# Kernel optimization log

Measured on AMD Instinct MI355X. Metric: run time of the kernel, lower is better.

The kernel has to match this reference:

```python
import jax, jax.numpy as jnp
import numpy as np

NUM_CLASSES = 2
THRESHOLD = 0.35
NEGPOS_RATIO = 7
VARIANCES = (0.1, 0.2)
B, P, O = 64, 16800, 64  # batch, num_priors, num_objs per image


def point_form(pr):
    # cxcywh -> xyxy
    return jnp.concatenate([pr[:, :2] - pr[:, 2:] / 2, pr[:, :2] + pr[:, 2:] / 2], axis=1)


def jaccard(a, b):
    # a: [A,4] xyxy, b: [Bx,4] xyxy -> IoU [A,Bx]
    lt = jnp.maximum(a[:, None, :2], b[None, :, :2])
    rb = jnp.minimum(a[:, None, 2:], b[None, :, 2:])
    wh = jnp.clip(rb - lt, 0.0)
    inter = wh[..., 0] * wh[..., 1]
    area_a = ((a[:, 2] - a[:, 0]) * (a[:, 3] - a[:, 1]))[:, None]
    area_b = ((b[:, 2] - b[:, 0]) * (b[:, 3] - b[:, 1]))[None, :]
    return inter / (area_a + area_b - inter)


def encode(matched, priors):
    # matched xyxy [P,4], priors cxcywh [P,4]
    g_cxcy = (matched[:, :2] + matched[:, 2:]) / 2 - priors[:, :2]
    g_cxcy = g_cxcy / (VARIANCES[0] * priors[:, 2:])
    g_wh = (matched[:, 2:] - matched[:, :2]) / priors[:, 2:]
    g_wh = jnp.log(g_wh) / VARIANCES[1]
    return jnp.concatenate([g_cxcy, g_wh], axis=1)


def encode_landm(matched, priors):
    # matched [P,10] -> [P,5,2]
    m = matched.reshape(-1, 5, 2)
    g = (m - priors[:, None, :2]) / (VARIANCES[0] * priors[:, None, 2:])
    return g.reshape(-1, 10)


def match_one(truths, labels, landms, priors):
    # truths [O,4], labels [O], landms [O,10]
    overlaps = jaccard(truths, point_form(priors))  # [O,P]
    best_prior_overlap = overlaps.max(axis=1)       # per-gt best IoU
    best_prior_idx = overlaps.argmax(axis=1)
    valid_gt = best_prior_overlap >= 0.2
    best_truth_overlap = overlaps.max(axis=0)       # per-prior best IoU
    best_truth_idx = overlaps.argmax(axis=0)
    # index_fill(2) only for valid gts (best_prior_idx_filter)
    bto = best_truth_overlap.at[best_prior_idx].set(
        jnp.where(valid_gt, 2.0, best_truth_overlap[best_prior_idx]))
    # ensure every gt keeps its best prior
    bti = best_truth_idx.at[best_prior_idx].set(jnp.arange(truths.shape[0]))
    matches = truths[bti]                  # [P,4]
    conf = labels[bti]                     # [P]
    conf = jnp.where(bto < THRESHOLD, 0.0, conf)
    loc = encode(matches, priors)
    landm = encode_landm(landms[bti], priors)
    return loc, conf, landm


def smooth_l1_sum(x, mask):
    ax = jnp.abs(x)
    v = jnp.where(ax < 1.0, 0.5 * ax * ax, ax - 0.5)
    return (v * mask).sum()


def setup_inputs() -> dict:
    key = jax.random.key(0)
    k1, k2, k3, k4, k5, k6, k7, k8 = jax.random.split(key, 8)
    loc_data = jax.random.normal(k1, (B, P, 4), jnp.float32)
    conf_data = jax.random.normal(k2, (B, P, NUM_CLASSES), jnp.float32)
    landm_data = jax.random.normal(k3, (B, P, 10), jnp.float32)
    # priors: cx,cy in (0,1), w,h in (0.02,0.22)
    cxy = jax.random.uniform(k4, (P, 2), jnp.float32)
    wh = jax.random.uniform(k5, (P, 2), jnp.float32) * 0.2 + 0.02
    priors = jnp.concatenate([cxy, wh], axis=1)
    # targets: valid corner boxes + landmarks + label in {1,-1}
    xy1 = jax.random.uniform(k6, (B, O, 2), jnp.float32) * 0.6
    bwh = jax.random.uniform(k7, (B, O, 2), jnp.float32) * 0.3 + 0.05
    boxes = jnp.concatenate([xy1, xy1 + bwh], axis=-1)
    lms = jax.random.uniform(k8, (B, O, 10), jnp.float32)
    lab = jnp.where(jax.random.uniform(jax.random.fold_in(key, 9), (B, O, 1)) < 0.3, -1.0, 1.0)
    targets = jnp.concatenate([boxes, lms, lab], axis=-1)
    return {"loc_data": loc_data, "conf_data": conf_data, "landm_data": landm_data,
            "priors": priors, "targets": targets}


def reference(loc_data, conf_data, landm_data, priors, targets):
    num = loc_data.shape[0]
    num_priors = priors.shape[0]
    truths = targets[:, :, :4]
    landms = targets[:, :, 4:14]
    labels = targets[:, :, -1]
    loc_t, conf_t, landm_t = jax.vmap(match_one, in_axes=(0, 0, 0, None))(
        truths, labels, landms, priors)  # [B,P,4], [B,P], [B,P,10]

    # landmark loss over conf_t > 0
    pos1 = conf_t > 0
    num_pos_landm = pos1.astype(jnp.int32).sum(axis=1, keepdims=True)
    N1 = jnp.maximum(num_pos_landm.sum().astype(jnp.float32), 1.0)
    loss_landm = smooth_l1_sum(landm_data - landm_t, pos1[..., None].astype(landm_data.dtype))

    # localization loss over conf_t != 0 ; conf_t[pos] = 1
    pos = conf_t != 0
    conf_t01 = jnp.where(pos, 1, 0)  # int {0,1}
    loss_l = smooth_l1_sum(loc_data - loc_t, pos[..., None].astype(loc_data.dtype))

    # hard negative mining on per-prior CE loss (global-max log_sum_exp, as in source)
    batch_conf = conf_data.reshape(-1, NUM_CLASSES)
    x_max = batch_conf.max()
    lse = jnp.log(jnp.exp(batch_conf - x_max).sum(axis=1, keepdims=True)) + x_max
    gathered = jnp.take_along_axis(batch_conf, conf_t01.reshape(-1, 1), axis=1)
    loss_c = (lse - gathered).reshape(num, -1)  # [B,P]; positives NOT zeroed (as in source)
    loss_idx = jnp.argsort(-loss_c, axis=1)
    idx_rank = jnp.argsort(loss_idx, axis=1)
    num_pos = pos.astype(jnp.int32).sum(axis=1, keepdims=True)  # [B,1]
    num_neg = jnp.minimum(NEGPOS_RATIO * num_pos, num_priors - 1)
    neg = idx_rank < num_neg  # [B,P]
    neg_pos = pos | neg

    # cross-entropy (sum) over selected pos+neg priors
    logp = jax.nn.log_softmax(conf_data, axis=-1)  # [B,P,C]
    ce = -jnp.take_along_axis(logp, conf_t01[..., None], axis=-1)[..., 0]
    loss_c_final = (ce * neg_pos.astype(ce.dtype)).sum()

    N = jnp.maximum(num_pos.sum().astype(jnp.float32), 1.0)
    return (loss_l / N, loss_c_final / N, loss_landm / N1)
```

## Files before the change

kernel.cpp:

```cpp
#include <hip/hip_runtime.h>
#include <math.h>

#define BN 64
#define PN 16800
#define ON 64
#define THRESH 0.35f
#define NEGPOS 7
#define GX 66
#define NBLK (BN * GX)
#define GXB 33
#define NB_BT (BN * GXB)
#define TG 4

__device__ __forceinline__ unsigned f2key(float f) {
  unsigned u = __float_as_uint(f);
  return (u & 0x80000000u) ? ~u : (u | 0x80000000u);
}
__device__ __forceinline__ float key2f(unsigned k) {
  unsigned u = (k & 0x80000000u) ? (k & 0x7FFFFFFFu) : ~k;
  return __uint_as_float(u);
}

struct Acc {
  unsigned xmax_key;
};

__device__ __forceinline__ float sl1(float d) {
  float a = fabsf(d);
  return (a < 1.f) ? 0.5f * a * a : a - 0.5f;
}

__global__ void k_best_truth(const float* __restrict__ priors,
                             const float* __restrict__ targets,
                             const float* __restrict__ conf,
                             float* __restrict__ bto, int* __restrict__ bti,
                             unsigned* __restrict__ bmax) {
  int b = blockIdx.y;
  int tid = threadIdx.x;
  int p0 = blockIdx.x * 512 + tid;
  int p1 = p0 + 256;
  bool v1 = p1 < PN;

  __shared__ float4 tbox[ON];
  __shared__ float tarea[ON];
  if (tid < ON) {
    const float* tg = &targets[((long)b * ON + tid) * 15];
    float4 bx = make_float4(tg[0], tg[1], tg[2], tg[3]);
    tbox[tid] = bx;
    tarea[tid] = (bx.z - bx.x) * (bx.w - bx.y);
  }
  __syncthreads();

  float2 c0 = reinterpret_cast<const float2*>(conf)[(long)b * PN + p0];
  float cmax = fmaxf(c0.x, c0.y);
  if (v1) {
    float2 c1 = reinterpret_cast<const float2*>(conf)[(long)b * PN + p1];
    cmax = fmaxf(cmax, fmaxf(c1.x, c1.y));
  }

  float4 prA = reinterpret_cast<const float4*>(priors)[p0];
  float4 prB = reinterpret_cast<const float4*>(priors)[v1 ? p1 : p0];
  float ax1A = prA.x - prA.z * 0.5f, ay1A = prA.y - prA.w * 0.5f;
  float ax2A = prA.x + prA.z * 0.5f, ay2A = prA.y + prA.w * 0.5f;
  float abA = (ax2A - ax1A) * (ay2A - ay1A);
  float ax1B = prB.x - prB.z * 0.5f, ay1B = prB.y - prB.w * 0.5f;
  float ax2B = prB.x + prB.z * 0.5f, ay2B = prB.y + prB.w * 0.5f;
  float abB = (ax2B - ax1B) * (ay2B - ay1B);

  float biA = -1.f, buA = 1.f, biB = -1.f, buB = 1.f;
  int idA = 0, idB = 0;
#pragma unroll 4
  for (int t = 0; t < ON; t++) {
    float4 a = tbox[t];
    float aa = tarea[t];
    {
      float lx = fmaxf(a.x, ax1A), ly = fmaxf(a.y, ay1A);
      float rx = fminf(a.z, ax2A), ry = fminf(a.w, ay2A);
      float w = fmaxf(rx - lx, 0.f), h = fmaxf(ry - ly, 0.f);
      float inter = w * h;
      float uni = aa + abA - inter;
      if (inter * buA > biA * uni) { biA = inter; buA = uni; idA = t; }
    }
    {
      float lx = fmaxf(a.x, ax1B), ly = fmaxf(a.y, ay1B);
      float rx = fminf(a.z, ax2B), ry = fminf(a.w, ay2B);
      float w = fmaxf(rx - lx, 0.f), h = fmaxf(ry - ly, 0.f);
      float inter = w * h;
      float uni = aa + abB - inter;
      if (inter * buB > biB * uni) { biB = inter; buB = uni; idB = t; }
    }
  }
  bto[b * PN + p0] = biA / buA;
  bti[b * PN + p0] = idA;
  if (v1) {
    bto[b * PN + p1] = biB / buB;
    bti[b * PN + p1] = idB;
  }

  for (int off = 32; off; off >>= 1) cmax = fmaxf(cmax, __shfl_down(cmax, off));
  __shared__ float wm[4];
  if ((tid & 63) == 0) wm[tid >> 6] = cmax;
  __syncthreads();
  if (tid == 0)
    bmax[b * GXB + blockIdx.x] = f2key(fmaxf(fmaxf(wm[0], wm[1]), fmaxf(wm[2], wm[3])));
}

__global__ void k_best_prior(const float* __restrict__ priors,
                             const float* __restrict__ targets,
                             float* __restrict__ bpo, int* __restrict__ bpi) {
  int bx = blockIdx.x;
  int b = bx >> 4;
  int t0 = (bx & 15) * TG;
  int tid = threadIdx.x;
  float ax1[TG], ay1[TG], ax2[TG], ay2[TG], area_a[TG];
#pragma unroll
  for (int i = 0; i < TG; i++) {
    const float* tg = &targets[((long)b * ON + t0 + i) * 15];
    ax1[i] = tg[0]; ay1[i] = tg[1]; ax2[i] = tg[2]; ay2[i] = tg[3];
    area_a[i] = (ax2[i] - ax1[i]) * (ay2[i] - ay1[i]);
  }
  float bi[TG], bu[TG]; int bp[TG];
#pragma unroll
  for (int i = 0; i < TG; i++) { bi[i] = -1.f; bu[i] = 1.f; bp[i] = 0x7FFFFFFF; }
  for (int p = tid; p < PN; p += 256) {
    float4 pr = reinterpret_cast<const float4*>(priors)[p];
    float px1 = pr.x - pr.z * 0.5f, py1 = pr.y - pr.w * 0.5f;
    float px2 = pr.x + pr.z * 0.5f, py2 = pr.y + pr.w * 0.5f;
    float area_b = (px2 - px1) * (py2 - py1);
#pragma unroll
    for (int i = 0; i < TG; i++) {
      float lx = fmaxf(ax1[i], px1), ly = fmaxf(ay1[i], py1);
      float rx = fminf(ax2[i], px2), ry = fminf(ay2[i], py2);
      float w = fmaxf(rx - lx, 0.f), h = fmaxf(ry - ly, 0.f);
      float inter = w * h;
      float uni = area_a[i] + area_b - inter;
      if (inter * bu[i] > bi[i] * uni) { bi[i] = inter; bu[i] = uni; bp[i] = p; }
    }
  }
#pragma unroll
  for (int off = 1; off < 64; off <<= 1) {
#pragma unroll
    for (int i = 0; i < TG; i++) {
      float oi = __shfl_xor(bi[i], off), ou = __shfl_xor(bu[i], off);
      int op = __shfl_xor(bp[i], off);
      float a = oi * bu[i], c = bi[i] * ou;
      if (a > c || (a == c && op < bp[i])) { bi[i] = oi; bu[i] = ou; bp[i] = op; }
    }
  }
  __shared__ float si[TG][4], su[TG][4];
  __shared__ int sp[TG][4];
  int w = tid >> 6;
  if ((tid & 63) == 0) {
#pragma unroll
    for (int i = 0; i < TG; i++) { si[i][w] = bi[i]; su[i][w] = bu[i]; sp[i][w] = bp[i]; }
  }
  __syncthreads();
  if (tid < TG) {
    float fi = si[tid][0], fu = su[tid][0]; int fp = sp[tid][0];
    for (int ww = 1; ww < 4; ww++) {
      float a = si[tid][ww] * fu, c = fi * su[tid][ww];
      if (a > c || (a == c && sp[tid][ww] < fp)) { fi = si[tid][ww]; fu = su[tid][ww]; fp = sp[tid][ww]; }
    }
    bpo[(long)b * ON + t0 + tid] = fi / fu;
    bpi[(long)b * ON + t0 + tid] = fp;
  }
}

__global__ void k_scatter(const unsigned* __restrict__ bmax,
                          const float* __restrict__ bpo, const int* __restrict__ bpi,
                          float* __restrict__ bto, int* __restrict__ bti, Acc* acc) {
  int tid = threadIdx.x;
  if (blockIdx.x == 16) {
    unsigned mk = 0;
    for (int i = tid; i < NB_BT; i += 256) { unsigned v = bmax[i]; if (v > mk) mk = v; }
    for (int off = 1; off < 64; off <<= 1) {
      unsigned o = (unsigned)__shfl_xor((int)mk, off);
      if (o > mk) mk = o;
    }
    __shared__ unsigned wm[4];
    if ((tid & 63) == 0) wm[tid >> 6] = mk;
    __syncthreads();
    if (tid == 0) {
      unsigned m = wm[0];
      if (wm[1] > m) m = wm[1];
      if (wm[2] > m) m = wm[2];
      if (wm[3] > m) m = wm[3];
      acc->xmax_key = m;
    }
    return;
  }
  int row = blockIdx.x * 4 + (tid >> 6);
  int t = tid & 63;
  int q = bpi[row * ON + t];
  bool valid = bpo[row * ON + t] >= 0.2f;
  bool dupLater = false;
  for (int j = 0; j < 64; j++) {
    int ij = __shfl(q, j);
    if (j > t && ij == q) dupLater = true;
  }
  if (!dupLater) {
    bti[(long)row * PN + q] = t;
    if (valid) bto[(long)row * PN + q] = 2.0f;
  }
}

__global__ void k_encode(const float* __restrict__ loc_data,
                         const float* __restrict__ conf_data,
                         const float* __restrict__ landm_data,
                         const float* __restrict__ priors,
                         const float* __restrict__ targets,
                         const float* __restrict__ bto, const int* __restrict__ bti,
                         float* __restrict__ lossc, unsigned char* __restrict__ posf,
                         const Acc* __restrict__ acc,
                         float* __restrict__ part_l, float* __restrict__ part_lm,
                         int* __restrict__ np_part, int* __restrict__ np1_part) {
  int b = blockIdx.y;
  int p = blockIdx.x * 256 + threadIdx.x;
  int bid = b * GX + blockIdx.x;
  __shared__ float tgs[ON * 15];
  for (int i = threadIdx.x; i < ON * 15; i += 256)
    tgs[i] = targets[(long)b * ON * 15 + i];
  __syncthreads();
  float sum_l = 0.f, sum_lm = 0.f;
  int cp = 0, cp1 = 0;
  if (p < PN) {
    int t = bti[b * PN + p];
    float ov = bto[b * PN + p];
    const float* tg = &tgs[t * 15];
    float label = tg[14];
    float conf = (ov < THRESH) ? 0.f : label;
    bool pos = (conf != 0.f);
    bool pos1 = (conf > 0.f);
    float4 pr = reinterpret_cast<const float4*>(priors)[p];
    if (pos) {
      float m0 = tg[0], m1 = tg[1], m2 = tg[2], m3 = tg[3];
      float g0 = ((m0 + m2) * 0.5f - pr.x) / (0.1f * pr.z);
      float g1 = ((m1 + m3) * 0.5f - pr.y) / (0.1f * pr.w);
      float g2 = logf((m2 - m0) / pr.z) / 0.2f;
      float g3 = logf((m3 - m1) / pr.w) / 0.2f;
      const float* ld = &loc_data[((long)b * PN + p) * 4];
      sum_l = sl1(ld[0] - g0) + sl1(ld[1] - g1) + sl1(ld[2] - g2) + sl1(ld[3] - g3);
      cp = 1;
    }
    if (pos1) {
      const float* lm = &landm_data[((long)b * PN + p) * 10];
      for (int i = 0; i < 5; i++) {
        float gx = (tg[4 + 2 * i] - pr.x) / (0.1f * pr.z);
        float gy = (tg[5 + 2 * i] - pr.y) / (0.1f * pr.w);
        sum_lm += sl1(lm[2 * i] - gx) + sl1(lm[2 * i + 1] - gy);
      }
      cp1 = 1;
    }
    float2 c2 = reinterpret_cast<const float2*>(conf_data)[(long)b * PN + p];
    float xmax = key2f(acc->xmax_key);
    float lse = logf(expf(c2.x - xmax) + expf(c2.y - xmax)) + xmax;
    lossc[b * PN + p] = lse - (pos ? c2.y : c2.x);
    posf[b * PN + p] = pos ? 1 : 0;
  }
  for (int off = 32; off; off >>= 1) {
    sum_l += __shfl_down(sum_l, off);
    sum_lm += __shfl_down(sum_lm, off);
    cp += __shfl_down(cp, off);
    cp1 += __shfl_down(cp1, off);
  }
  __shared__ float sl4[4], slm4[4];
  __shared__ int sp4[4], sp14[4];
  int w = threadIdx.x >> 6;
  if ((threadIdx.x & 63) == 0) { sl4[w] = sum_l; slm4[w] = sum_lm; sp4[w] = cp; sp14[w] = cp1; }
  __syncthreads();
  if (threadIdx.x == 0) {
    part_l[bid] = sl4[0] + sl4[1] + sl4[2] + sl4[3];
    part_lm[bid] = slm4[0] + slm4[1] + slm4[2] + slm4[3];
    np_part[bid] = sp4[0] + sp4[1] + sp4[2] + sp4[3];
    np1_part[bid] = sp14[0] + sp14[1] + sp14[2] + sp14[3];
  }
}

__global__ void __launch_bounds__(1024) k_select_sum(const float* __restrict__ lossc,
                                                     const unsigned char* __restrict__ posf,
                                                     const int* __restrict__ np_part,
                                                     float* __restrict__ part_c) {
  int b = blockIdx.x;
  int tid = threadIdx.x;
  __shared__ unsigned hist[256], suf[256];
  __shared__ unsigned s_chosen, s_rem;
  __shared__ int s_np;
  const float* row = &lossc[(long)b * PN];
  const unsigned char* prow = &posf[(long)b * PN];

  if (tid == 0) s_np = 0;
  __syncthreads();
  if (tid < GX) atomicAdd(&s_np, np_part[b * GX + tid]);
  __syncthreads();
  int np = s_np;
  long k = (long)NEGPOS * np;
  if (k > PN - 1) k = PN - 1;

  unsigned T = 0xFFFFFFFFu, R = 0, C = 0;
  if (k > 0) {
    unsigned prefix = 0, remaining = (unsigned)k, lastC = 0;
    for (int pass = 0; pass < 4; pass++) {
      int shift = 24 - pass * 8;
      if (tid < 256) hist[tid] = 0;
      __syncthreads();
      unsigned hmask = (pass == 0) ? 0u : (0xFFFFFFFFu << (shift + 8));
      for (int p = tid; p < PN; p += 1024) {
        unsigned key = f2key(row[p]);
        if (((key ^ prefix) & hmask) == 0)
          atomicAdd(&hist[(key >> shift) & 255], 1u);
      }
      __syncthreads();
      if (tid < 256) suf[tid] = hist[tid];
      __syncthreads();
      for (int off = 1; off < 256; off <<= 1) {
        unsigned tv = 0;
        if (tid < 256 && tid + off < 256) tv = suf[tid + off];
        __syncthreads();
        if (tid < 256) suf[tid] += tv;
        __syncthreads();
      }
      if (tid < 256) {
        unsigned nextS = (tid < 255) ? suf[tid + 1] : 0;
        if (suf[tid] >= remaining && nextS < remaining) {
          s_chosen = (unsigned)tid;
          s_rem = remaining - nextS;
        }
      }
      __syncthreads();
      prefix |= s_chosen << shift;
      remaining = s_rem;
      if (pass == 3) lastC = hist[s_chosen];
      __syncthreads();
    }
    T = prefix; R = remaining; C = lastC;
  }

  float s = 0.f;
  bool fastTies = (R > 0 && C == R);
  for (int p = tid; p < PN; p += 1024) {
    bool pos = prow[p] != 0;
    float v = row[p];
    unsigned key = f2key(v);
    bool sel = pos || (R > 0 && (key > T || (key == T && fastTies)));
    if (sel) s += v;
  }
  if (R > 0 && C != R && tid < 64) {
    unsigned running = 0;
    for (int base = 0; base < PN; base += 64) {
      int p = base + tid;
      bool tie = false, pos = false;
      float v = 0.f;
      if (p < PN) {
        v = row[p];
        tie = (f2key(v) == T);
        pos = prow[p] != 0;
      }
      unsigned long long m = __ballot(tie);
      if (tie) {
        unsigned rank = running + (unsigned)__popcll(m & ((1ull << tid) - 1));
        if (rank < R && !pos) s += v;
      }
      running += (unsigned)__popcll(m);
    }
  }
  for (int off = 32; off; off >>= 1) s += __shfl_down(s, off);
  __shared__ float ws[16];
  if ((tid & 63) == 0) ws[tid >> 6] = s;
  __syncthreads();
  if (tid == 0) {
    float tot = 0.f;
    for (int i = 0; i < 16; i++) tot += ws[i];
    part_c[b] = tot;
  }
}

__global__ void k_final(const float* __restrict__ part_l, const float* __restrict__ part_lm,
                        const float* __restrict__ part_c,
                        const int* __restrict__ np_part, const int* __restrict__ np1_part,
                        float* __restrict__ out) {
  float sl = 0.f, slm = 0.f, sc = 0.f;
  int np = 0, np1 = 0;
  for (int i = threadIdx.x; i < NBLK; i += 256) {
    sl += part_l[i]; slm += part_lm[i];
    np += np_part[i]; np1 += np1_part[i];
  }
  if (threadIdx.x < BN) sc = part_c[threadIdx.x];
  for (int off = 32; off; off >>= 1) {
    sl += __shfl_down(sl, off); slm += __shfl_down(slm, off); sc += __shfl_down(sc, off);
    np += __shfl_down(np, off); np1 += __shfl_down(np1, off);
  }
  __shared__ float a[4], bsh[4], c[4];
  __shared__ int d[4], e[4];
  int w = threadIdx.x >> 6;
  if ((threadIdx.x & 63) == 0) { a[w] = sl; bsh[w] = slm; c[w] = sc; d[w] = np; e[w] = np1; }
  __syncthreads();
  if (threadIdx.x == 0) {
    float N = fmaxf((float)(d[0] + d[1] + d[2] + d[3]), 1.f);
    float N1 = fmaxf((float)(e[0] + e[1] + e[2] + e[3]), 1.f);
    out[0] = (a[0] + a[1] + a[2] + a[3]) / N;
    out[1] = (c[0] + c[1] + c[2] + c[3]) / N;
    out[2] = (bsh[0] + bsh[1] + bsh[2] + bsh[3]) / N1;
  }
}

extern "C" void kernel_launch(void* const* d_in, const int* in_sizes, int n_in,
                              void* d_out, int out_size, void* d_ws, size_t ws_size,
                              hipStream_t stream) {
  const float* loc_data = (const float*)d_in[0];
  const float* conf_data = (const float*)d_in[1];
  const float* landm_data = (const float*)d_in[2];
  const float* priors = (const float*)d_in[3];
  const float* targets = (const float*)d_in[4];
  float* out = (float*)d_out;

  char* ws = (char*)d_ws;
  const size_t SZ = (size_t)BN * PN * 4;
  size_t off = 0;
  float* lossc = (float*)(ws + off); off += SZ;
  float* bto = (float*)(ws + off); off += SZ;
  int* bti = (int*)(ws + off); off += SZ;
  unsigned char* posf = (unsigned char*)(ws + off); off += (size_t)BN * PN;
  off = (off + 15) & ~(size_t)15;
  float* bpo = (float*)(ws + off); off += (size_t)BN * ON * 4;
  int* bpi = (int*)(ws + off); off += (size_t)BN * ON * 4;
  unsigned* bmax = (unsigned*)(ws + off); off += NB_BT * 4;
  float* part_l = (float*)(ws + off); off += NBLK * 4;
  float* part_lm = (float*)(ws + off); off += NBLK * 4;
  float* part_c = (float*)(ws + off); off += BN * 4;
  int* np_part = (int*)(ws + off); off += NBLK * 4;
  int* np1_part = (int*)(ws + off); off += NBLK * 4;
  Acc* acc = (Acc*)(ws + off); off += sizeof(Acc);

  dim3 gbt(GXB, BN);
  dim3 gbp(GX, BN);

  k_best_truth<<<gbt, 256, 0, stream>>>(priors, targets, conf_data, bto, bti, bmax);
  k_best_prior<<<BN * (ON / TG), 256, 0, stream>>>(priors, targets, bpo, bpi);
  k_scatter<<<17, 256, 0, stream>>>(bmax, bpo, bpi, bto, bti, acc);
  k_encode<<<gbp, 256, 0, stream>>>(loc_data, conf_data, landm_data, priors, targets,
                                    bto, bti, lossc, posf, acc,
                                    part_l, part_lm, np_part, np1_part);
  k_select_sum<<<BN, 1024, 0, stream>>>(lossc, posf, np_part, part_c);
  k_final<<<1, 256, 0, stream>>>(part_l, part_lm, part_c, np_part, np1_part, out);
}
```

Baseline: 230.9 us.

## Fuse matching kernels with last-block tickets and switch to 3-pass radix select

New measurement: 462.9 us. 2x slower.

```diff
diff --git a/kernel.cpp b/kernel.cpp
--- a/kernel.cpp
+++ b/kernel.cpp
@@ -9,7 +9,9 @@
 #define GX 66
 #define NBLK (BN * GX)
 #define GXB 33
-#define NB_BT (BN * GXB)
+#define NBT (BN * GXB)
+#define NBP 1024
+#define K1_TOTAL (NBT + NBP)
 #define TG 4
 
 __device__ __forceinline__ unsigned f2key(float f) {
@@ -20,187 +22,148 @@
   unsigned u = (k & 0x80000000u) ? (k & 0x7FFFFFFFu) : ~k;
   return __uint_as_float(u);
 }
-
-struct Acc {
-  unsigned xmax_key;
-};
-
 __device__ __forceinline__ float sl1(float d) {
   float a = fabsf(d);
   return (a < 1.f) ? 0.5f * a * a : a - 0.5f;
 }
 
-__global__ void k_best_truth(const float* __restrict__ priors,
-                             const float* __restrict__ targets,
-                             const float* __restrict__ conf,
-                             float* __restrict__ bto, int* __restrict__ bti,
-                             unsigned* __restrict__ bmax) {
-  int b = blockIdx.y;
+__global__ void k_match(const float* __restrict__ priors,
+                        const float* __restrict__ targets,
+                        float* __restrict__ bto, int* __restrict__ bti,
+                        float* __restrict__ bpo, int* __restrict__ bpi,
+                        unsigned* __restrict__ ticket) {
+  int bid = blockIdx.x;
   int tid = threadIdx.x;
-  int p0 = blockIdx.x * 512 + tid;
-  int p1 = p0 + 256;
-  bool v1 = p1 < PN;
-
-  __shared__ float4 tbox[ON];
-  __shared__ float tarea[ON];
-  if (tid < ON) {
-    const float* tg = &targets[((long)b * ON + tid) * 15];
-    float4 bx = make_float4(tg[0], tg[1], tg[2], tg[3]);
-    tbox[tid] = bx;
-    tarea[tid] = (bx.z - bx.x) * (bx.w - bx.y);
-  }
-  __syncthreads();
-
-  float2 c0 = reinterpret_cast<const float2*>(conf)[(long)b * PN + p0];
-  float cmax = fmaxf(c0.x, c0.y);
-  if (v1) {
-    float2 c1 = reinterpret_cast<const float2*>(conf)[(long)b * PN + p1];
-    cmax = fmaxf(cmax, fmaxf(c1.x, c1.y));
-  }
-
-  float4 prA = reinterpret_cast<const float4*>(priors)[p0];
-  float4 prB = reinterpret_cast<const float4*>(priors)[v1 ? p1 : p0];
-  float ax1A = prA.x - prA.z * 0.5f, ay1A = prA.y - prA.w * 0.5f;
-  float ax2A = prA.x + prA.z * 0.5f, ay2A = prA.y + prA.w * 0.5f;
-  float abA = (ax2A - ax1A) * (ay2A - ay1A);
-  float ax1B = prB.x - prB.z * 0.5f, ay1B = prB.y - prB.w * 0.5f;
-  float ax2B = prB.x + prB.z * 0.5f, ay2B = prB.y + prB.w * 0.5f;
-  float abB = (ax2B - ax1B) * (ay2B - ay1B);
-
-  float biA = -1.f, buA = 1.f, biB = -1.f, buB = 1.f;
-  int idA = 0, idB = 0;
-#pragma unroll 4
-  for (int t = 0; t < ON; t++) {
-    float4 a = tbox[t];
-    float aa = tarea[t];
-    {
-      float lx = fmaxf(a.x, ax1A), ly = fmaxf(a.y, ay1A);
-      float rx = fminf(a.z, ax2A), ry = fminf(a.w, ay2A);
-      float w = fmaxf(rx - lx, 0.f), h = fmaxf(ry - ly, 0.f);
-      float inter = w * h;
-      float uni = aa + abA - inter;
-      if (inter * buA > biA * uni) { biA = inter; buA = uni; idA = t; }
-    }
-    {
-      float lx = fmaxf(a.x, ax1B), ly = fmaxf(a.y, ay1B);
-      float rx = fminf(a.z, ax2B), ry = fminf(a.w, ay2B);
-      float w = fmaxf(rx - lx, 0.f), h = fmaxf(ry - ly, 0.f);
-      float inter = w * h;
-      float uni = aa + abB - inter;
-      if (inter * buB > biB * uni) { biB = inter; buB = uni; idB = t; }
-    }
-  }
-  bto[b * PN + p0] = biA / buA;
-  bti[b * PN + p0] = idA;
-  if (v1) {
-    bto[b * PN + p1] = biB / buB;
-    bti[b * PN + p1] = idB;
-  }
-
-  for (int off = 32; off; off >>= 1) cmax = fmaxf(cmax, __shfl_down(cmax, off));
-  __shared__ float wm[4];
-  if ((tid & 63) == 0) wm[tid >> 6] = cmax;
-  __syncthreads();
-  if (tid == 0)
-    bmax[b * GXB + blockIdx.x] = f2key(fmaxf(fmaxf(wm[0], wm[1]), fmaxf(wm[2], wm[3])));
-}
-
-__global__ void k_best_prior(const float* __restrict__ priors,
-                             const float* __restrict__ targets,
-                             float* __restrict__ bpo, int* __restrict__ bpi) {
-  int bx = blockIdx.x;
-  int b = bx >> 4;
-  int t0 = (bx & 15) * TG;
-  int tid = threadIdx.x;
-  float ax1[TG], ay1[TG], ax2[TG], ay2[TG], area_a[TG];
-#pragma unroll
-  for (int i = 0; i < TG; i++) {
-    const float* tg = &targets[((long)b * ON + t0 + i) * 15];
-    ax1[i] = tg[0]; ay1[i] = tg[1]; ax2[i] = tg[2]; ay2[i] = tg[3];
-    area_a[i] = (ax2[i] - ax1[i]) * (ay2[i] - ay1[i]);
-  }
-  float bi[TG], bu[TG]; int bp[TG];
-#pragma unroll
-  for (int i = 0; i < TG; i++) { bi[i] = -1.f; bu[i] = 1.f; bp[i] = 0x7FFFFFFF; }
-  for (int p = tid; p < PN; p += 256) {
-    float4 pr = reinterpret_cast<const float4*>(priors)[p];
-    float px1 = pr.x - pr.z * 0.5f, py1 = pr.y - pr.w * 0.5f;
-    float px2 = pr.x + pr.z * 0.5f, py2 = pr.y + pr.w * 0.5f;
-    float area_b = (px2 - px1) * (py2 - py1);
+  __shared__ float si[TG][4], su[TG][4];
+  __shared__ int spx[TG][4];
+  __shared__ int lastFlag;
+
+  if (bid < NBT) {
+    int b = bid / GXB;
+    int xb = bid - b * GXB;
+    int p0 = xb * 512 + tid;
+    int p1 = p0 + 256;
+    bool v1 = p1 < PN;
+    float4 prA = reinterpret_cast<const float4*>(priors)[p0];
+    float4 prB = reinterpret_cast<const float4*>(priors)[v1 ? p1 : p0];
+    float px1A = prA.x - prA.z * 0.5f, py1A = prA.y - prA.w * 0.5f;
+    float px2A = prA.x + prA.z * 0.5f, py2A = prA.y + prA.w * 0.5f;
+    float abA = (px2A - px1A) * (py2A - py1A);
+    float px1B = prB.x - prB.z * 0.5f, py1B = prB.y - prB.w * 0.5f;
+    float px2B = prB.x + prB.z * 0.5f, py2B = prB.y + prB.w * 0.5f;
+    float abB = (px2B - px1B) * (py2B - py1B);
+    const float* tgb = &targets[(long)b * ON * 15];
+    float biA = -1.f, buA = 1.f, biB = -1.f, buB = 1.f;
+    int idA = 0, idB = 0;
+#pragma unroll 16
+    for (int t = 0; t < ON; t++) {
+      float x1 = tgb[t * 15 + 0], y1 = tgb[t * 15 + 1];
+      float x2 = tgb[t * 15 + 2], y2 = tgb[t * 15 + 3];
+      float aa = (x2 - x1) * (y2 - y1);
+      {
+        float lx = fmaxf(x1, px1A), ly = fmaxf(y1, py1A);
+        float rx = fminf(x2, px2A), ry = fminf(y2, py2A);
+        float w = fmaxf(rx - lx, 0.f), h = fmaxf(ry - ly, 0.f);
+        float inter = w * h;
+        float uni = aa + abA - inter;
+        if (inter * buA > biA * uni) { biA = inter; buA = uni; idA = t; }
+      }
+      {
+        float lx = fmaxf(x1, px1B), ly = fmaxf(y1, py1B);
+        float rx = fminf(x2, px2B), ry = fminf(y2, py2B);
+        float w = fmaxf(rx - lx, 0.f), h = fmaxf(ry - ly, 0.f);
+        float inter = w * h;
+        float uni = aa + abB - inter;
+        if (inter * buB > biB * uni) { biB = inter; buB = uni; idB = t; }
+      }
+    }
+    bto[b * PN + p0] = biA / buA;
+    bti[b * PN + p0] = idA;
+    if (v1) {
+      bto[b * PN + p1] = biB / buB;
+      bti[b * PN + p1] = idB;
+    }
+  } else {
+    int id2 = bid - NBT;
+    int b = id2 >> 4;
+    int t0 = (id2 & 15) * TG;
+    float ax1[TG], ay1[TG], ax2[TG], ay2[TG], area_a[TG];
 #pragma unroll
     for (int i = 0; i < TG; i++) {
-      float lx = fmaxf(ax1[i], px1), ly = fmaxf(ay1[i], py1);
-      float rx = fminf(ax2[i], px2), ry = fminf(ay2[i], py2);
-      float w = fmaxf(rx - lx, 0.f), h = fmaxf(ry - ly, 0.f);
-      float inter = w * h;
-      float uni = area_a[i] + area_b - inter;
-      if (inter * bu[i] > bi[i] * uni) { bi[i] = inter; bu[i] = uni; bp[i] = p; }
-    }
-  }
-#pragma unroll
-  for (int off = 1; off < 64; off <<= 1) {
-#pragma unroll
-    for (int i = 0; i < TG; i++) {
-      float oi = __shfl_xor(bi[i], off), ou = __shfl_xor(bu[i], off);
-      int op = __shfl_xor(bp[i], off);
-      float a = oi * bu[i], c = bi[i] * ou;
-      if (a > c || (a == c && op < bp[i])) { bi[i] = oi; bu[i] = ou; bp[i] = op; }
-    }
-  }
-  __shared__ float si[TG][4], su[TG][4];
-  __shared__ int sp[TG][4];
-  int w = tid >> 6;
-  if ((tid & 63) == 0) {
-#pragma unroll
-    for (int i = 0; i < TG; i++) { si[i][w] = bi[i]; su[i][w] = bu[i]; sp[i][w] = bp[i]; }
-  }
-  __syncthreads();
-  if (tid < TG) {
-    float fi = si[tid][0], fu = su[tid][0]; int fp = sp[tid][0];
-    for (int ww = 1; ww < 4; ww++) {
-      float a = si[tid][ww] * fu, c = fi * su[tid][ww];
-      if (a > c || (a == c && sp[tid][ww] < fp)) { fi = si[tid][ww]; fu = su[tid][ww]; fp = sp[tid][ww]; }
-    }
-    bpo[(long)b * ON + t0 + tid] = fi / fu;
-    bpi[(long)b * ON + t0 + tid] = fp;
-  }
-}
-
-__global__ void k_scatter(const unsigned* __restrict__ bmax,
-                          const float* __restrict__ bpo, const int* __restrict__ bpi,
-                          float* __restrict__ bto, int* __restrict__ bti, Acc* acc) {
-  int tid = threadIdx.x;
-  if (blockIdx.x == 16) {
-    unsigned mk = 0;
-    for (int i = tid; i < NB_BT; i += 256) { unsigned v = bmax[i]; if (v > mk) mk = v; }
+      const float* tg = &targets[((long)b * ON + t0 + i) * 15];
+      ax1[i] = tg[0]; ay1[i] = tg[1]; ax2[i] = tg[2]; ay2[i] = tg[3];
+      area_a[i] = (ax2[i] - ax1[i]) * (ay2[i] - ay1[i]);
+    }
+    float bi[TG], bu[TG]; int bp[TG];
+#pragma unroll
+    for (int i = 0; i < TG; i++) { bi[i] = -1.f; bu[i] = 1.f; bp[i] = 0x7FFFFFFF; }
+    for (int p = tid; p < PN; p += 256) {
+      float4 pr = reinterpret_cast<const float4*>(priors)[p];
+      float px1 = pr.x - pr.z * 0.5f, py1 = pr.y - pr.w * 0.5f;
+      float px2 = pr.x + pr.z * 0.5f, py2 = pr.y + pr.w * 0.5f;
+      float area_b = (px2 - px1) * (py2 - py1);
+#pragma unroll
+      for (int i = 0; i < TG; i++) {
+        float lx = fmaxf(ax1[i], px1), ly = fmaxf(ay1[i], py1);
+        float rx = fminf(ax2[i], px2), ry = fminf(ay2[i], py2);
+        float w = fmaxf(rx - lx, 0.f), h = fmaxf(ry - ly, 0.f);
+        float inter = w * h;
+        float uni = area_a[i] + area_b - inter;
+        if (inter * bu[i] > bi[i] * uni) { bi[i] = inter; bu[i] = uni; bp[i] = p; }
+      }
+    }
+#pragma unroll
     for (int off = 1; off < 64; off <<= 1) {
-      unsigned o = (unsigned)__shfl_xor((int)mk, off);
-      if (o > mk) mk = o;
-    }
-    __shared__ unsigned wm[4];
-    if ((tid & 63) == 0) wm[tid >> 6] = mk;
-    __syncthreads();
-    if (tid == 0) {
-      unsigned m = wm[0];
-      if (wm[1] > m) m = wm[1];
-      if (wm[2] > m) m = wm[2];
-      if (wm[3] > m) m = wm[3];
-      acc->xmax_key = m;
-    }
-    return;
-  }
-  int row = blockIdx.x * 4 + (tid >> 6);
-  int t = tid & 63;
-  int q = bpi[row * ON + t];
-  bool valid = bpo[row * ON + t] >= 0.2f;
-  bool dupLater = false;
-  for (int j = 0; j < 64; j++) {
-    int ij = __shfl(q, j);
-    if (j > t && ij == q) dupLater = true;
-  }
-  if (!dupLater) {
-    bti[(long)row * PN + q] = t;
-    if (valid) bto[(long)row * PN + q] = 2.0f;
+#pragma unroll
+      for (int i = 0; i < TG; i++) {
+        float oi = __shfl_xor(bi[i], off), ou = __shfl_xor(bu[i], off);
+        int op = __shfl_xor(bp[i], off);
+        float a = oi * bu[i], c = bi[i] * ou;
+        if (a > c || (a == c && op < bp[i])) { bi[i] = oi; bu[i] = ou; bp[i] = op; }
+      }
+    }
+    int w = tid >> 6;
+    if ((tid & 63) == 0) {
+#pragma unroll
+      for (int i = 0; i < TG; i++) { si[i][w] = bi[i]; su[i][w] = bu[i]; spx[i][w] = bp[i]; }
+    }
+    __syncthreads();
+    if (tid < TG) {
+      float fi = si[tid][0], fu = su[tid][0]; int fp = spx[tid][0];
+      for (int ww = 1; ww < 4; ww++) {
+        float a = si[tid][ww] * fu, c = fi * su[tid][ww];
+        if (a > c || (a == c && spx[tid][ww] < fp)) { fi = si[tid][ww]; fu = su[tid][ww]; fp = spx[tid][ww]; }
+      }
+      bpo[(long)b * ON + t0 + tid] = fi / fu;
+      bpi[(long)b * ON + t0 + tid] = fp;
+    }
+  }
+
+  __threadfence();
+  if (tid == 0) {
+    unsigned old = atomicAdd(ticket, 1u);
+    lastFlag = (old == (unsigned)(K1_TOTAL - 1)) ? 1 : 0;
+  }
+  __syncthreads();
+  if (lastFlag) {
+    __threadfence();
+    int lane = tid & 63;
+    int w = tid >> 6;
+    for (int g = 0; g < 16; g++) {
+      int row = g * 4 + w;
+      int q = bpi[row * ON + lane];
+      float ov = bpo[row * ON + lane];
+      bool valid = ov >= 0.2f;
+      bool dupLater = false;
+      for (int j = 0; j < 64; j++) {
+        int ij = __shfl(q, j);
+        if (j > lane && ij == q) dupLater = true;
+      }
+      if (!dupLater) {
+        bti[(long)row * PN + q] = lane;
+        if (valid) bto[(long)row * PN + q] = 2.0f;
+      }
+    }
   }
 }
 
@@ -211,7 +174,6 @@
                          const float* __restrict__ targets,
                          const float* __restrict__ bto, const int* __restrict__ bti,
                          float* __restrict__ lossc, unsigned char* __restrict__ posf,
-                         const Acc* __restrict__ acc,
                          float* __restrict__ part_l, float* __restrict__ part_lm,
                          int* __restrict__ np_part, int* __restrict__ np1_part) {
   int b = blockIdx.y;
@@ -228,32 +190,33 @@
     float ov = bto[b * PN + p];
     const float* tg = &tgs[t * 15];
     float label = tg[14];
-    float conf = (ov < THRESH) ? 0.f : label;
-    bool pos = (conf != 0.f);
-    bool pos1 = (conf > 0.f);
+    bool pos = ov >= THRESH;
+    bool pos1 = pos && (label > 0.f);
     float4 pr = reinterpret_cast<const float4*>(priors)[p];
     if (pos) {
+      float rz = 1.0f / pr.z, rw = 1.0f / pr.w;
       float m0 = tg[0], m1 = tg[1], m2 = tg[2], m3 = tg[3];
-      float g0 = ((m0 + m2) * 0.5f - pr.x) / (0.1f * pr.z);
-      float g1 = ((m1 + m3) * 0.5f - pr.y) / (0.1f * pr.w);
-      float g2 = logf((m2 - m0) / pr.z) / 0.2f;
-      float g3 = logf((m3 - m1) / pr.w) / 0.2f;
+      float g0 = ((m0 + m2) * 0.5f - pr.x) * rz * 10.f;
+      float g1 = ((m1 + m3) * 0.5f - pr.y) * rw * 10.f;
+      float g2 = __logf((m2 - m0) * rz) * 5.f;
+      float g3 = __logf((m3 - m1) * rw) * 5.f;
       const float* ld = &loc_data[((long)b * PN + p) * 4];
       sum_l = sl1(ld[0] - g0) + sl1(ld[1] - g1) + sl1(ld[2] - g2) + sl1(ld[3] - g3);
       cp = 1;
-    }
-    if (pos1) {
-      const float* lm = &landm_data[((long)b * PN + p) * 10];
-      for (int i = 0; i < 5; i++) {
-        float gx = (tg[4 + 2 * i] - pr.x) / (0.1f * pr.z);
-        float gy = (tg[5 + 2 * i] - pr.y) / (0.1f * pr.w);
-        sum_lm += sl1(lm[2 * i] - gx) + sl1(lm[2 * i + 1] - gy);
-      }
-      cp1 = 1;
+      if (pos1) {
+        const float* lm = &landm_data[((long)b * PN + p) * 10];
+#pragma unroll
+        for (int i = 0; i < 5; i++) {
+          float gx = (tg[4 + 2 * i] - pr.x) * rz * 10.f;
+          float gy = (tg[5 + 2 * i] - pr.y) * rw * 10.f;
+          sum_lm += sl1(lm[2 * i] - gx) + sl1(lm[2 * i + 1] - gy);
+        }
+        cp1 = 1;
+      }
     }
     float2 c2 = reinterpret_cast<const float2*>(conf_data)[(long)b * PN + p];
-    float xmax = key2f(acc->xmax_key);
-    float lse = logf(expf(c2.x - xmax) + expf(c2.y - xmax)) + xmax;
+    float m = fmaxf(c2.x, c2.y);
+    float lse = m + __logf(__expf(c2.x - m) + __expf(c2.y - m));
     lossc[b * PN + p] = lse - (pos ? c2.y : c2.x);
     posf[b * PN + p] = pos ? 1 : 0;
   }
@@ -276,15 +239,22 @@
   }
 }
 
-__global__ void __launch_bounds__(1024) k_select_sum(const float* __restrict__ lossc,
-                                                     const unsigned char* __restrict__ posf,
-                                                     const int* __restrict__ np_part,
-                                                     float* __restrict__ part_c) {
+__global__ void __launch_bounds__(1024) k_select(const float* __restrict__ lossc,
+                                                 const unsigned char* __restrict__ posf,
+                                                 const int* __restrict__ np_part,
+                                                 const int* __restrict__ np1_part,
+                                                 const float* __restrict__ part_l,
+                                                 const float* __restrict__ part_lm,
+                                                 float* __restrict__ part_c,
+                                                 unsigned* __restrict__ ticket,
+                                                 float* __restrict__ out) {
   int b = blockIdx.x;
   int tid = threadIdx.x;
-  __shared__ unsigned hist[256], suf[256];
-  __shared__ unsigned s_chosen, s_rem;
+  __shared__ unsigned bins[4096];
+  __shared__ unsigned gs[1025];
+  __shared__ unsigned s_d, s_rem;
   __shared__ int s_np;
+  __shared__ int lastF;
   const float* row = &lossc[(long)b * PN];
   const unsigned char* prow = &posf[(long)b * PN];
 
@@ -293,113 +263,165 @@
   if (tid < GX) atomicAdd(&s_np, np_part[b * GX + tid]);
   __syncthreads();
   int np = s_np;
-  long k = (long)NEGPOS * np;
+  int k = NEGPOS * np;
   if (k > PN - 1) k = PN - 1;
-
-  unsigned T = 0xFFFFFFFFu, R = 0, C = 0;
-  if (k > 0) {
-    unsigned prefix = 0, remaining = (unsigned)k, lastC = 0;
-    for (int pass = 0; pass < 4; pass++) {
-      int shift = 24 - pass * 8;
-      if (tid < 256) hist[tid] = 0;
-      __syncthreads();
-      unsigned hmask = (pass == 0) ? 0u : (0xFFFFFFFFu << (shift + 8));
-      for (int p = tid; p < PN; p += 1024) {
-        unsigned key = f2key(row[p]);
-        if (((key ^ prefix) & hmask) == 0)
-          atomicAdd(&hist[(key >> shift) & 255], 1u);
-      }
-      __syncthreads();
-      if (tid < 256) suf[tid] = hist[tid];
-      __syncthreads();
-      for (int off = 1; off < 256; off <<= 1) {
-        unsigned tv = 0;
-        if (tid < 256 && tid + off < 256) tv = suf[tid + off];
-        __syncthreads();
-        if (tid < 256) suf[tid] += tv;
-        __syncthreads();
-      }
-      if (tid < 256) {
-        unsigned nextS = (tid < 255) ? suf[tid + 1] : 0;
-        if (suf[tid] >= remaining && nextS < remaining) {
-          s_chosen = (unsigned)tid;
-          s_rem = remaining - nextS;
-        }
-      }
-      __syncthreads();
-      prefix |= s_chosen << shift;
-      remaining = s_rem;
-      if (pass == 3) lastC = hist[s_chosen];
-      __syncthreads();
-    }
-    T = prefix; R = remaining; C = lastC;
-  }
-
-  float s = 0.f;
-  bool fastTies = (R > 0 && C == R);
+  bool haveNeg = (k > 0);
+
+  unsigned T = 0, R = 0, C = 0;
+  if (haveNeg) {
+    unsigned rem = (unsigned)k;
+    for (int i = tid; i < 4096; i += 1024) bins[i] = 0;
+    __syncthreads();
+    for (int p = tid; p < PN; p += 1024) atomicAdd(&bins[f2key(row[p]) >> 20], 1u);
+    __syncthreads();
+    unsigned l0 = bins[4 * tid], l1 = bins[4 * tid + 1], l2 = bins[4 * tid + 2], l3 = bins[4 * tid + 3];
+    gs[tid] = l0 + l1 + l2 + l3;
+    if (tid == 0) gs[1024] = 0;
+    __syncthreads();
+    for (int off = 1; off < 1024; off <<= 1) {
+      unsigned v = (tid + off < 1024) ? gs[tid + off] : 0;
+      __syncthreads();
+      gs[tid] += v;
+      __syncthreads();
+    }
+    {
+      unsigned nx = gs[tid + 1];
+      if (gs[tid] >= rem && nx < rem) {
+        unsigned run = nx, cc; int d;
+        if (run + l3 >= rem) { d = 3; cc = l3; }
+        else { run += l3;
+          if (run + l2 >= rem) { d = 2; cc = l2; }
+          else { run += l2;
+            if (run + l1 >= rem) { d = 1; cc = l1; }
+            else { run += l1; d = 0; cc = l0; } } }
+        (void)cc;
+        s_d = 4 * (unsigned)tid + (unsigned)d;
+        s_rem = rem - run;
+      }
+    }
+    __syncthreads();
+    unsigned d0 = s_d; rem = s_rem;
+    __syncthreads();
+    bins[tid] = 0;
+    __syncthreads();
+    for (int p = tid; p < PN; p += 1024) {
+      unsigned key = f2key(row[p]);
+      if ((key >> 20) == d0) atomicAdd(&bins[(key >> 10) & 1023], 1u);
+    }
+    __syncthreads();
+    gs[tid] = bins[tid];
+    if (tid == 0) gs[1024] = 0;
+    __syncthreads();
+    for (int off = 1; off < 1024; off <<= 1) {
+      unsigned v = (tid + off < 1024) ? gs[tid + off] : 0;
+      __syncthreads();
+      gs[tid] += v;
+      __syncthreads();
+    }
+    {
+      unsigned nx = gs[tid + 1];
+      if (gs[tid] >= rem && nx < rem) { s_d = (unsigned)tid; s_rem = rem - nx; }
+    }
+    __syncthreads();
+    unsigned d1 = s_d; rem = s_rem;
+    unsigned pref = (d0 << 10) | d1;
+    __syncthreads();
+    bins[tid] = 0;
+    __syncthreads();
+    for (int p = tid; p < PN; p += 1024) {
+      unsigned key = f2key(row[p]);
+      if ((key >> 10) == pref) atomicAdd(&bins[key & 1023], 1u);
+    }
+    __syncthreads();
+    gs[tid] = bins[tid];
+    if (tid == 0) gs[1024] = 0;
+    __syncthreads();
+    for (int off = 1; off < 1024; off <<= 1) {
+      unsigned v = (tid + off < 1024) ? gs[tid + off] : 0;
+      __syncthreads();
+      gs[tid] += v;
+      __syncthreads();
+    }
+    {
+      unsigned nx = gs[tid + 1];
+      if (gs[tid] >= rem && nx < rem) { s_d = (unsigned)tid; s_rem = rem - nx; }
+    }
+    __syncthreads();
+    unsigned d2 = s_d;
+    R = s_rem;
+    C = bins[d2];
+    T = (pref << 10) | d2;
+  }
+
+  float acc = 0.f;
+  unsigned ptc = 0;
   for (int p = tid; p < PN; p += 1024) {
+    float v = row[p];
     bool pos = prow[p] != 0;
-    float v = row[p];
     unsigned key = f2key(v);
-    bool sel = pos || (R > 0 && (key > T || (key == T && fastTies)));
-    if (sel) s += v;
-  }
-  if (R > 0 && C != R && tid < 64) {
+    if (pos) acc += v;
+    else if (haveNeg && key > T) acc += v;
+    if (haveNeg && pos && key == T) ptc++;
+  }
+  if (haveNeg && C != R && tid < 64) {
     unsigned running = 0;
     for (int base = 0; base < PN; base += 64) {
       int p = base + tid;
       bool tie = false, pos = false;
       float v = 0.f;
-      if (p < PN) {
-        v = row[p];
-        tie = (f2key(v) == T);
-        pos = prow[p] != 0;
-      }
+      if (p < PN) { v = row[p]; tie = (f2key(v) == T); pos = prow[p] != 0; }
       unsigned long long m = __ballot(tie);
       if (tie) {
         unsigned rank = running + (unsigned)__popcll(m & ((1ull << tid) - 1));
-        if (rank < R && !pos) s += v;
+        if (rank < R && !pos) acc += v;
       }
       running += (unsigned)__popcll(m);
     }
   }
-  for (int off = 32; off; off >>= 1) s += __shfl_down(s, off);
-  __shared__ float ws[16];
-  if ((tid & 63) == 0) ws[tid >> 6] = s;
+  for (int off = 32; off; off >>= 1) {
+    acc += __shfl_down(acc, off);
+    ptc += __shfl_down(ptc, off);
+  }
+  __shared__ float wsum[16];
+  __shared__ unsigned wpt[16];
+  if ((tid & 63) == 0) { wsum[tid >> 6] = acc; wpt[tid >> 6] = ptc; }
   __syncthreads();
   if (tid == 0) {
-    float tot = 0.f;
-    for (int i = 0; i < 16; i++) tot += ws[i];
+    float tot = 0.f; unsigned pt = 0;
+    for (int i = 0; i < 16; i++) { tot += wsum[i]; pt += wpt[i]; }
+    if (haveNeg && C == R) tot += (float)(C - pt) * key2f(T);
     part_c[b] = tot;
   }
-}
-
-__global__ void k_final(const float* __restrict__ part_l, const float* __restrict__ part_lm,
-                        const float* __restrict__ part_c,
-                        const int* __restrict__ np_part, const int* __restrict__ np1_part,
-                        float* __restrict__ out) {
-  float sl = 0.f, slm = 0.f, sc = 0.f;
-  int np = 0, np1 = 0;
-  for (int i = threadIdx.x; i < NBLK; i += 256) {
-    sl += part_l[i]; slm += part_lm[i];
-    np += np_part[i]; np1 += np1_part[i];
-  }
-  if (threadIdx.x < BN) sc = part_c[threadIdx.x];
-  for (int off = 32; off; off >>= 1) {
-    sl += __shfl_down(sl, off); slm += __shfl_down(slm, off); sc += __shfl_down(sc, off);
-    np += __shfl_down(np, off); np1 += __shfl_down(np1, off);
-  }
-  __shared__ float a[4], bsh[4], c[4];
-  __shared__ int d[4], e[4];
-  int w = threadIdx.x >> 6;
-  if ((threadIdx.x & 63) == 0) { a[w] = sl; bsh[w] = slm; c[w] = sc; d[w] = np; e[w] = np1; }
-  __syncthreads();
-  if (threadIdx.x == 0) {
-    float N = fmaxf((float)(d[0] + d[1] + d[2] + d[3]), 1.f);
-    float N1 = fmaxf((float)(e[0] + e[1] + e[2] + e[3]), 1.f);
-    out[0] = (a[0] + a[1] + a[2] + a[3]) / N;
-    out[1] = (c[0] + c[1] + c[2] + c[3]) / N;
-    out[2] = (bsh[0] + bsh[1] + bsh[2] + bsh[3]) / N1;
+
+  __threadfence();
+  if (tid == 0) lastF = (atomicAdd(ticket, 1u) == (unsigned)(BN - 1)) ? 1 : 0;
+  __syncthreads();
+  if (lastF) {
+    __threadfence();
+    float sl = 0.f, slm = 0.f, sc = 0.f;
+    int npT = 0, np1T = 0;
+    for (int i = tid; i < NBLK; i += 1024) {
+      sl += part_l[i]; slm += part_lm[i];
+      npT += np_part[i]; np1T += np1_part[i];
+    }
+    if (tid < BN) sc = part_c[tid];
+    for (int off = 32; off; off >>= 1) {
+      sl += __shfl_down(sl, off); slm += __shfl_down(slm, off); sc += __shfl_down(sc, off);
+      npT += __shfl_down(npT, off); np1T += __shfl_down(np1T, off);
+    }
+    __shared__ float fa[16], fb[16], fc[16];
+    __shared__ int ia[16], ib[16];
+    if ((tid & 63) == 0) { fa[tid >> 6] = sl; fb[tid >> 6] = slm; fc[tid >> 6] = sc; ia[tid >> 6] = npT; ib[tid >> 6] = np1T; }
+    __syncthreads();
+    if (tid == 0) {
+      float tsl = 0, tslm = 0, tsc = 0; int tnp = 0, tnp1 = 0;
+      for (int i = 0; i < 16; i++) { tsl += fa[i]; tslm += fb[i]; tsc += fc[i]; tnp += ia[i]; tnp1 += ib[i]; }
+      float N = fmaxf((float)tnp, 1.f);
+      float N1 = fmaxf((float)tnp1, 1.f);
+      out[0] = tsl / N;
+      out[1] = tsc / N;
+      out[2] = tslm / N1;
+    }
   }
 }
 
@@ -423,23 +445,20 @@
   off = (off + 15) & ~(size_t)15;
   float* bpo = (float*)(ws + off); off += (size_t)BN * ON * 4;
   int* bpi = (int*)(ws + off); off += (size_t)BN * ON * 4;
-  unsigned* bmax = (unsigned*)(ws + off); off += NB_BT * 4;
   float* part_l = (float*)(ws + off); off += NBLK * 4;
   float* part_lm = (float*)(ws + off); off += NBLK * 4;
   float* part_c = (float*)(ws + off); off += BN * 4;
   int* np_part = (int*)(ws + off); off += NBLK * 4;
   int* np1_part = (int*)(ws + off); off += NBLK * 4;
-  Acc* acc = (Acc*)(ws + off); off += sizeof(Acc);
-
-  dim3 gbt(GXB, BN);
+  unsigned* tickets = (unsigned*)(ws + off); off += 2 * sizeof(unsigned);
+
+  hipMemsetAsync(tickets, 0, 2 * sizeof(unsigned), stream);
+
+  k_match<<<K1_TOTAL, 256, 0, stream>>>(priors, targets, bto, bti, bpo, bpi, &tickets[0]);
   dim3 gbp(GX, BN);
-
-  k_best_truth<<<gbt, 256, 0, stream>>>(priors, targets, conf_data, bto, bti, bmax);
-  k_best_prior<<<BN * (ON / TG), 256, 0, stream>>>(priors, targets, bpo, bpi);
-  k_scatter<<<17, 256, 0, stream>>>(bmax, bpo, bpi, bto, bti, acc);
   k_encode<<<gbp, 256, 0, stream>>>(loc_data, conf_data, landm_data, priors, targets,
-                                    bto, bti, lossc, posf, acc,
+                                    bto, bti, lossc, posf,
                                     part_l, part_lm, np_part, np1_part);
-  k_select_sum<<<BN, 1024, 0, stream>>>(lossc, posf, np_part, part_c);
-  k_final<<<1, 256, 0, stream>>>(part_l, part_lm, part_c, np_part, np1_part, out);
-}
+  k_select<<<BN, 1024, 0, stream>>>(lossc, posf, np_part, np1_part, part_l, part_lm,
+                                    part_c, &tickets[1], out);
+}
```
